# Kernel tuning notes

Measured on AMD Instinct MI355X. Metric: run time of the kernel, lower is better.

Reference implementation:

```python
import jax, jax.numpy as jnp
import numpy as np

B, F_, H, N, R = 4096, 16, 1280, 8, 64
TAU = 1.0  # taus[0] on first training step (tau_start)
EPS = 1e-12


def setup_inputs() -> dict:
    key = jax.random.key(0)
    kx, ku, kg, kd, kup = jax.random.split(key, 5)
    x = jax.random.normal(kx, (B, F_, H), dtype=jnp.float32)
    u = jax.random.uniform(ku, (B, N), dtype=jnp.float32)  # gumbel base noise
    stdv = 1.0 / np.sqrt(16 * H)
    gate_w = jax.random.uniform(kg, (N, 16 * H), minval=-stdv, maxval=stdv, dtype=jnp.float32)
    sigma = jnp.ones((), dtype=jnp.float32)
    down_w = jax.random.normal(kd, (N, R, H), dtype=jnp.float32) * (1.0 / R)
    # original inits up to zeros; use small noise so the output/grads are non-trivial
    up_w = jax.random.normal(kup, (N, H, R), dtype=jnp.float32) * 0.02
    return {"x": x, "u": u, "gate_w": gate_w, "sigma": sigma, "down_w": down_w, "up_w": up_w}


def _l2norm(a, axis):
    n = jnp.linalg.norm(a, axis=axis, keepdims=True)
    return a / jnp.maximum(n, EPS)


def reference(x, u, gate_w, sigma, down_w, up_w):
    # gate: cosine linear on flattened (f c)
    xf = x.reshape(x.shape[0], -1)                      # [B, 16H]
    logits = sigma * (_l2norm(xf, 1) @ _l2norm(gate_w, 1).T)  # [B, N]
    # gumbel-softmax with straight-through hard one-hot
    g = -jnp.log(-jnp.log(u + EPS) + EPS)
    y_soft = jax.nn.softmax((logits + g) / TAU, axis=-1)
    y_hard = jax.nn.one_hot(jnp.argmax(y_soft, axis=-1), N, dtype=y_soft.dtype)
    gates = y_hard + y_soft - jax.lax.stop_gradient(y_soft)  # [B, N]
    # fused batched LoRA: down-proj, gate-weight, up-proj+expert-reduce
    mid = jnp.einsum('bfc,nrc->bfnr', x, down_w)        # [B, F, N, R]
    gmid = mid * gates[:, None, :, None]
    out = jnp.einsum('bfnr,nhr->bfh', gmid, up_w)       # [B, F, H]
    return out
```

## Files before the change

kernel.cpp:

```cpp
#include <hip/hip_runtime.h>

#define EPSF 1e-12f

typedef __bf16 bf16x8 __attribute__((ext_vector_type(8)));
typedef float  f32x4  __attribute__((ext_vector_type(4)));

static __device__ __forceinline__ unsigned short f2b(float f) {
  unsigned int u = __float_as_uint(f);
  u += 0x7fffu + ((u >> 16) & 1u);
  return (unsigned short)(u >> 16);
}

static __device__ __forceinline__ bf16x8 as_bf(uint4 v) {
  union { uint4 u; bf16x8 b; } c; c.u = v; return c.b;
}

__global__ __launch_bounds__(256) void prep_cvt(const float4* __restrict__ dw4,
                                                const float4* __restrict__ uw4,
                                                ushort4* __restrict__ dwb4,
                                                ushort4* __restrict__ uwb4) {
  const int o = blockIdx.x * 256 + threadIdx.x;
  const int e = o / 20480, o1 = o - e * 20480;
  {
    const int rt = o1 / 5120, o2 = o1 - rt * 5120;
    const int s = o2 >> 7, r2 = o2 & 127;
    const int ln = r2 >> 1, j0 = (r2 & 1) << 2;
    const int src = (rt * 16 + (ln & 15)) * 1280 + (s << 5) + ((ln >> 4) << 3) + j0;
    float4 v = dw4[(e * 81920 + src) >> 2];
    ushort4 t; t.x = f2b(v.x); t.y = f2b(v.y); t.z = f2b(v.z); t.w = f2b(v.w);
    dwb4[o] = t;
  }
  {
    const int tt = o1 >> 8, o3 = o1 & 255;
    const int s2 = o3 >> 7, r2 = o3 & 127;
    const int ln = r2 >> 1, j0 = (r2 & 1) << 2;
    const int src = (tt * 16 + (ln & 15)) * 64 + (s2 << 5) + ((ln >> 4) << 3) + j0;
    float4 v = uw4[(e * 81920 + src) >> 2];
    ushort4 t; t.x = f2b(v.x); t.y = f2b(v.y); t.z = f2b(v.z); t.w = f2b(v.w);
    uwb4[o] = t;
  }
}

__global__ __launch_bounds__(256) void k1_gate(const float* __restrict__ x,
                                               const float* __restrict__ u,
                                               const float* __restrict__ gate_w,
                                               const float* __restrict__ sigma_p,
                                               int* __restrict__ sel) {
  __shared__ float gwch[8 * 1280];
  const int tid = threadIdx.x, lane = tid & 63, w = tid >> 6;
  const int row = blockIdx.x * 4 + w;
  const float4* x4 = (const float4*)x + (size_t)row * 5120;
  const float4* gw4 = (const float4*)gate_w;
  float4* gwch4 = (float4*)gwch;

  float ss = 0.f;
  float dot[8];
#pragma unroll
  for (int n = 0; n < 8; ++n) dot[n] = 0.f;
  float gws0 = 0.f, gws1 = 0.f;

  for (int ch = 0; ch < 16; ++ch) {
    float4 gv[2][5];
#pragma unroll
    for (int rr = 0; rr < 2; ++rr) {
      const int n = w + 4 * rr;
#pragma unroll
      for (int p = 0; p < 5; ++p)
        gv[rr][p] = gw4[(size_t)n * 5120 + ch * 320 + p * 64 + lane];
    }
#pragma unroll
    for (int p = 0; p < 5; ++p) {
      float4 a = gv[0][p], b = gv[1][p];
      gwch4[(w)*320 + p * 64 + lane] = a;
      gwch4[(w + 4) * 320 + p * 64 + lane] = b;
      gws0 += a.x * a.x + a.y * a.y + a.z * a.z + a.w * a.w;
      gws1 += b.x * b.x + b.y * b.y + b.z * b.z + b.w * b.w;
    }
    __syncthreads();
    float4 xv[5];
#pragma unroll
    for (int p = 0; p < 5; ++p) xv[p] = x4[ch * 320 + p * 64 + lane];
#pragma unroll
    for (int p = 0; p < 5; ++p) {
      float4 v = xv[p];
      ss += v.x * v.x + v.y * v.y + v.z * v.z + v.w * v.w;
#pragma unroll
      for (int n = 0; n < 8; ++n) {
        float4 g = gwch4[n * 320 + p * 64 + lane];
        dot[n] += v.x * g.x + v.y * g.y + v.z * g.z + v.w * g.w;
      }
    }
    __syncthreads();
  }

#pragma unroll
  for (int off = 32; off; off >>= 1) {
    ss += __shfl_xor(ss, off);
    gws0 += __shfl_xor(gws0, off);
    gws1 += __shfl_xor(gws1, off);
#pragma unroll
    for (int n = 0; n < 8; ++n) dot[n] += __shfl_xor(dot[n], off);
  }
  if (lane == 0) { gwch[w] = gws0; gwch[w + 4] = gws1; }
  __syncthreads();
  if (lane == 0) {
    const float sg = *sigma_p;
    const float inv_xn = 1.f / fmaxf(sqrtf(ss), EPSF);
    float best = -3.4e38f; int se = 0;
#pragma unroll
    for (int n = 0; n < 8; ++n) {
      const float gwi = 1.f / fmaxf(sqrtf(gwch[n]), EPSF);
      const float logit = sg * (dot[n] * inv_xn * gwi);
      const float uu = u[(size_t)row * 8 + n];
      const float g = -logf(-logf(uu + EPSF) + EPSF);
      const float y = logit + g;
      if (y > best) { best = y; se = n; }
    }
    sel[row] = se;
  }
}

__global__ __launch_bounds__(256) void k2_lora(const float* __restrict__ x,
                                               const int* __restrict__ sel,
                                               const unsigned short* __restrict__ dwb,
                                               const unsigned short* __restrict__ uwb,
                                               float* __restrict__ out) {
  __shared__ __align__(16) unsigned short xs[40 * 512];
  __shared__ __align__(16) unsigned short mids[16 * 88];
  const int b = blockIdx.x;
  const int tid = threadIdx.x, lane = tid & 63, w = tid >> 6;
  const int l16 = lane & 15, q = lane >> 4;
  const int e = sel[b];

  const float4* xb4 = (const float4*)x + (size_t)b * 5120;
  const int c4b = l16 * 320 + q * 2;
#pragma unroll
  for (int t = 0; t < 10; ++t) {
    const int s = w + 4 * t;
    float4 v0 = xb4[c4b + s * 8];
    float4 v1 = xb4[c4b + s * 8 + 1];
    union { ushort4 h[2]; uint4 v; } pk;
    pk.h[0].x = f2b(v0.x); pk.h[0].y = f2b(v0.y); pk.h[0].z = f2b(v0.z); pk.h[0].w = f2b(v0.w);
    pk.h[1].x = f2b(v1.x); pk.h[1].y = f2b(v1.y); pk.h[1].z = f2b(v1.z); pk.h[1].w = f2b(v1.w);
    *(uint4*)&xs[s * 512 + lane * 8] = pk.v;
  }
  __syncthreads();

  const unsigned short* dwe = dwb + (size_t)(e * 4 + w) * 20480 + lane * 8;
  f32x4 acc = {0.f, 0.f, 0.f, 0.f};
#pragma unroll 8
  for (int s = 0; s < 40; ++s) {
    bf16x8 af = as_bf(*(const uint4*)&xs[s * 512 + lane * 8]);
    bf16x8 bf = as_bf(*(const uint4*)(dwe + (size_t)s * 512));
    acc = __builtin_amdgcn_mfma_f32_16x16x32_bf16(af, bf, acc, 0, 0, 0);
  }
#pragma unroll
  for (int j = 0; j < 4; ++j)
    mids[(q * 4 + j) * 88 + w * 16 + l16] = f2b(acc[j]);
  __syncthreads();

  bf16x8 a0 = as_bf(*(const uint4*)&mids[l16 * 88 + q * 8]);
  bf16x8 a1 = as_bf(*(const uint4*)&mids[l16 * 88 + 32 + q * 8]);
  const unsigned short* uwe = uwb + (size_t)e * 81920 + lane * 8;
  float* outb = out + (size_t)b * 20480 + q * 4 * 1280 + l16;
#pragma unroll 2
  for (int t = w; t < 80; t += 4) {
    const unsigned short* up = uwe + t * 1024;
    bf16x8 b0 = as_bf(*(const uint4*)up);
    bf16x8 b1 = as_bf(*(const uint4*)(up + 512));
    f32x4 o = {0.f, 0.f, 0.f, 0.f};
    o = __builtin_amdgcn_mfma_f32_16x16x32_bf16(a0, b0, o, 0, 0, 0);
    o = __builtin_amdgcn_mfma_f32_16x16x32_bf16(a1, b1, o, 0, 0, 0);
    float* op = outb + t * 16;
    op[0]    = o[0];
    op[1280] = o[1];
    op[2560] = o[2];
    op[3840] = o[3];
  }
}

extern "C" void kernel_launch(void* const* d_in, const int* in_sizes, int n_in,
                              void* d_out, int out_size, void* d_ws, size_t ws_size,
                              hipStream_t stream) {
  const float* x      = (const float*)d_in[0];
  const float* u      = (const float*)d_in[1];
  const float* gate_w = (const float*)d_in[2];
  const float* sigma  = (const float*)d_in[3];
  const float* down_w = (const float*)d_in[4];
  const float* up_w   = (const float*)d_in[5];
  float* out = (float*)d_out;

  int* sel = (int*)d_ws;
  unsigned short* dwb = (unsigned short*)((char*)d_ws + 16384);
  unsigned short* uwb = dwb + 655360;

  prep_cvt<<<640, 256, 0, stream>>>((const float4*)down_w, (const float4*)up_w,
                                    (ushort4*)dwb, (ushort4*)uwb);
  k1_gate<<<1024, 256, 0, stream>>>(x, u, gate_w, sigma, sel);
  k2_lora<<<4096, 256, 0, stream>>>(x, sel, dwb, uwb, out);
}
```

Measured before the change: 702.5 us.

## Emit bf16 copy of x from gate kernel and read it in LoRA kernel

The gate kernel, which already streams x in fp32, now also writes a bf16 copy of x into workspace. The LoRA kernel reads that bf16 copy straight from global memory into MFMA operands, which halves its x read and drops the LDS staging and conversion step. If the workspace is too small, a fallback path converts fp32 x in registers, also without LDS staging. The cost is an extra full-size bf16 write of x in the gate kernel, so total memory traffic may end up about the same as before.

```diff
diff --git a/kernel.cpp b/kernel.cpp
--- a/kernel.cpp
+++ b/kernel.cpp
@@ -45,7 +45,9 @@
                                                const float* __restrict__ u,
                                                const float* __restrict__ gate_w,
                                                const float* __restrict__ sigma_p,
-                                               int* __restrict__ sel) {
+                                               int* __restrict__ sel,
+                                               ushort4* __restrict__ xbf4,
+                                               const int wx) {
   __shared__ float gwch[8 * 1280];
   const int tid = threadIdx.x, lane = tid & 63, w = tid >> 6;
   const int row = blockIdx.x * 4 + w;
@@ -88,6 +90,14 @@
       for (int n = 0; n < 8; ++n) {
         float4 g = gwch4[n * 320 + p * 64 + lane];
         dot[n] += v.x * g.x + v.y * g.y + v.z * g.z + v.w * g.w;
+      }
+    }
+    if (wx) {
+#pragma unroll
+      for (int p = 0; p < 5; ++p) {
+        float4 v = xv[p];
+        ushort4 s4; s4.x = f2b(v.x); s4.y = f2b(v.y); s4.z = f2b(v.z); s4.w = f2b(v.w);
+        xbf4[(size_t)row * 5120 + ch * 320 + p * 64 + lane] = s4;
       }
     }
     __syncthreads();
@@ -120,37 +130,23 @@
   }
 }
 
-__global__ __launch_bounds__(256) void k2_lora(const float* __restrict__ x,
-                                               const int* __restrict__ sel,
-                                               const unsigned short* __restrict__ dwb,
-                                               const unsigned short* __restrict__ uwb,
-                                               float* __restrict__ out) {
-  __shared__ __align__(16) unsigned short xs[40 * 512];
+__global__ __launch_bounds__(256) void k2_lora_bf(const unsigned short* __restrict__ xbf,
+                                                  const int* __restrict__ sel,
+                                                  const unsigned short* __restrict__ dwb,
+                                                  const unsigned short* __restrict__ uwb,
+                                                  float* __restrict__ out) {
   __shared__ __align__(16) unsigned short mids[16 * 88];
   const int b = blockIdx.x;
   const int tid = threadIdx.x, lane = tid & 63, w = tid >> 6;
   const int l16 = lane & 15, q = lane >> 4;
   const int e = sel[b];
 
-  const float4* xb4 = (const float4*)x + (size_t)b * 5120;
-  const int c4b = l16 * 320 + q * 2;
-#pragma unroll
-  for (int t = 0; t < 10; ++t) {
-    const int s = w + 4 * t;
-    float4 v0 = xb4[c4b + s * 8];
-    float4 v1 = xb4[c4b + s * 8 + 1];
-    union { ushort4 h[2]; uint4 v; } pk;
-    pk.h[0].x = f2b(v0.x); pk.h[0].y = f2b(v0.y); pk.h[0].z = f2b(v0.z); pk.h[0].w = f2b(v0.w);
-    pk.h[1].x = f2b(v1.x); pk.h[1].y = f2b(v1.y); pk.h[1].z = f2b(v1.z); pk.h[1].w = f2b(v1.w);
-    *(uint4*)&xs[s * 512 + lane * 8] = pk.v;
-  }
-  __syncthreads();
-
+  const unsigned short* xrow = xbf + (size_t)b * 20480 + l16 * 1280 + q * 8;
   const unsigned short* dwe = dwb + (size_t)(e * 4 + w) * 20480 + lane * 8;
   f32x4 acc = {0.f, 0.f, 0.f, 0.f};
 #pragma unroll 8
   for (int s = 0; s < 40; ++s) {
-    bf16x8 af = as_bf(*(const uint4*)&xs[s * 512 + lane * 8]);
+    bf16x8 af = as_bf(*(const uint4*)(xrow + s * 32));
     bf16x8 bf = as_bf(*(const uint4*)(dwe + (size_t)s * 512));
     acc = __builtin_amdgcn_mfma_f32_16x16x32_bf16(af, bf, acc, 0, 0, 0);
   }
@@ -179,6 +175,56 @@
   }
 }
 
+__global__ __launch_bounds__(256) void k2_lora_f32(const float* __restrict__ x,
+                                                   const int* __restrict__ sel,
+                                                   const unsigned short* __restrict__ dwb,
+                                                   const unsigned short* __restrict__ uwb,
+                                                   float* __restrict__ out) {
+  __shared__ __align__(16) unsigned short mids[16 * 88];
+  const int b = blockIdx.x;
+  const int tid = threadIdx.x, lane = tid & 63, w = tid >> 6;
+  const int l16 = lane & 15, q = lane >> 4;
+  const int e = sel[b];
+
+  const float* xrow = x + (size_t)b * 20480 + l16 * 1280 + q * 8;
+  const unsigned short* dwe = dwb + (size_t)(e * 4 + w) * 20480 + lane * 8;
+  f32x4 acc = {0.f, 0.f, 0.f, 0.f};
+#pragma unroll 4
+  for (int s = 0; s < 40; ++s) {
+    float4 v0 = *(const float4*)(xrow + s * 32);
+    float4 v1 = *(const float4*)(xrow + s * 32 + 4);
+    union { ushort4 h[2]; uint4 v; } pk;
+    pk.h[0].x = f2b(v0.x); pk.h[0].y = f2b(v0.y); pk.h[0].z = f2b(v0.z); pk.h[0].w = f2b(v0.w);
+    pk.h[1].x = f2b(v1.x); pk.h[1].y = f2b(v1.y); pk.h[1].z = f2b(v1.z); pk.h[1].w = f2b(v1.w);
+    bf16x8 af = as_bf(pk.v);
+    bf16x8 bf = as_bf(*(const uint4*)(dwe + (size_t)s * 512));
+    acc = __builtin_amdgcn_mfma_f32_16x16x32_bf16(af, bf, acc, 0, 0, 0);
+  }
+#pragma unroll
+  for (int j = 0; j < 4; ++j)
+    mids[(q * 4 + j) * 88 + w * 16 + l16] = f2b(acc[j]);
+  __syncthreads();
+
+  bf16x8 a0 = as_bf(*(const uint4*)&mids[l16 * 88 + q * 8]);
+  bf16x8 a1 = as_bf(*(const uint4*)&mids[l16 * 88 + 32 + q * 8]);
+  const unsigned short* uwe = uwb + (size_t)e * 81920 + lane * 8;
+  float* outb = out + (size_t)b * 20480 + q * 4 * 1280 + l16;
+#pragma unroll 2
+  for (int t = w; t < 80; t += 4) {
+    const unsigned short* up = uwe + t * 1024;
+    bf16x8 b0 = as_bf(*(const uint4*)up);
+    bf16x8 b1 = as_bf(*(const uint4*)(up + 512));
+    f32x4 o = {0.f, 0.f, 0.f, 0.f};
+    o = __builtin_amdgcn_mfma_f32_16x16x32_bf16(a0, b0, o, 0, 0, 0);
+    o = __builtin_amdgcn_mfma_f32_16x16x32_bf16(a1, b1, o, 0, 0, 0);
+    float* op = outb + t * 16;
+    op[0]    = o[0];
+    op[1280] = o[1];
+    op[2560] = o[2];
+    op[3840] = o[3];
+  }
+}
+
 extern "C" void kernel_launch(void* const* d_in, const int* in_sizes, int n_in,
                               void* d_out, int out_size, void* d_ws, size_t ws_size,
                               hipStream_t stream) {
@@ -193,9 +239,15 @@
   int* sel = (int*)d_ws;
   unsigned short* dwb = (unsigned short*)((char*)d_ws + 16384);
   unsigned short* uwb = dwb + 655360;
+  unsigned short* xbf = (unsigned short*)((char*)d_ws + 2637824);
+  const size_t need = 2637824 + (size_t)4096 * 20480 * 2;
+  const int big = (ws_size >= need) ? 1 : 0;
 
   prep_cvt<<<640, 256, 0, stream>>>((const float4*)down_w, (const float4*)up_w,
                                     (ushort4*)dwb, (ushort4*)uwb);
-  k1_gate<<<1024, 256, 0, stream>>>(x, u, gate_w, sigma, sel);
-  k2_lora<<<4096, 256, 0, stream>>>(x, sel, dwb, uwb, out);
-}
+  k1_gate<<<1024, 256, 0, stream>>>(x, u, gate_w, sigma, sel, (ushort4*)xbf, big);
+  if (big)
+    k2_lora_bf<<<4096, 256, 0, stream>>>(xbf, sel, dwb, uwb, out);
+  else
+    k2_lora_f32<<<4096, 256, 0, stream>>>(x, sel, dwb, uwb, out);
+}
```

Result: slower. 760.5 us (+8.3%).
